# Optimization experiments

Hardware: AMD Instinct MI355X
Metric: run time of the kernel (lower is better)

## Reference

```python
import jax, jax.numpy as jnp
import numpy as np

N = 4096   # num_agents
F = 512    # feat_dim
P = 512    # phi_dim
A = 512    # aggr_dim
S = 6      # state_dim
H = 20     # MLP hidden width (hidden_layers=(20,20))


def _lstm(X, wih, whh, b):
    # torch.nn.LSTM single layer on an unbatched sequence X: [T, in] -> [T, hidden]
    pre = X @ wih + b  # [T, 4*hidden]
    Fh = whh.shape[0]
    def step(carry, p):
        h, c = carry
        g = p + h @ whh
        i, f, gg, o = jnp.split(g, 4, axis=-1)  # torch gate order: i, f, g, o
        c = jax.nn.sigmoid(f) * c + jax.nn.sigmoid(i) * jnp.tanh(gg)
        h = jax.nn.sigmoid(o) * jnp.tanh(c)
        return (h, c), h
    init = (jnp.zeros((Fh,), X.dtype), jnp.zeros((Fh,), X.dtype))
    _, hs = jax.lax.scan(step, init, pre)
    return hs


def setup_inputs():
    key = jax.random.key(0)
    ks = jax.random.split(key, 30)
    def rn(k, shape, s=0.05):
        return (jax.random.normal(k, shape) * s).astype(jnp.float32)
    x = jax.random.normal(ks[0], (N, F), dtype=jnp.float32)
    states = jax.random.normal(ks[1], (N, S), dtype=jnp.float32)
    # one comm link per agent (E == N, required by update()'s concat with x)
    src = jax.random.randint(ks[2], (N,), 0, N)
    dst = jnp.arange(N)
    inp = dict(x=x, states=states, src=src, dst=dst)
    inp["phi_w0"] = rn(ks[3], (4, F + S, H)); inp["phi_b0"] = rn(ks[4], (4, H))
    inp["phi_w1"] = rn(ks[5], (4, H, H));     inp["phi_b1"] = rn(ks[6], (4, H))
    inp["phi_w2"] = rn(ks[7], (4, H, P));     inp["phi_b2"] = rn(ks[8], (4, P))
    inp["tq_w"] = rn(ks[9], (4, P, A));  inp["tq_b"] = rn(ks[10], (4, A))
    inp["tk_w"] = rn(ks[11], (4, P, A)); inp["tk_b"] = rn(ks[12], (4, A))
    inp["tv_w"] = rn(ks[13], (4, P, A)); inp["tv_b"] = rn(ks[14], (4, A))
    inp["ts_w"] = rn(ks[15], (4, P, A)); inp["ts_b"] = rn(ks[16], (4, A))
    inp["wih0"] = rn(ks[17], (4, A + F, 4 * F)); inp["whh0"] = rn(ks[18], (4, F, 4 * F))
    inp["b0"] = rn(ks[19], (4, 4 * F))
    inp["wih1"] = rn(ks[20], (4, F, 4 * F)); inp["whh1"] = rn(ks[21], (4, F, 4 * F))
    inp["b1"] = rn(ks[22], (4, 4 * F))
    inp["cbf_w"] = rn(ks[23], (F, 1)); inp["cbf_b"] = rn(ks[24], (1,))
    return inp


def reference(x, states, src, dst, phi_w0, phi_b0, phi_w1, phi_b1, phi_w2, phi_b2,
              tq_w, tq_b, tk_w, tk_b, tv_w, tv_b, ts_w, ts_b,
              wih0, whh0, b0, wih1, whh1, b1, cbf_w, cbf_b):
    inv_sqrt_a = 1.0 / jnp.sqrt(jnp.float32(A))

    def gnn_layer(l, xin):
        # message: phi(concat(x_j, states_j - states_i))  (j = src, i = dst)
        msg = jnp.concatenate([xin[src], states[src] - states[dst]], axis=1)  # [E, F+S]
        h = jax.nn.relu(msg @ phi_w0[l] + phi_b0[l])
        h = jax.nn.relu(h @ phi_w1[l] + phi_b1[l])
        phi = h @ phi_w2[l] + phi_b2[l]  # [E, P]
        # aggregate: TransformerConv over message rows (E == N), heads=1
        q = phi @ tq_w[l] + tq_b[l]
        k = phi @ tk_w[l] + tk_b[l]
        v = phi @ tv_w[l] + tv_b[l]
        logits = jnp.sum(q[dst] * k[src], axis=-1) * inv_sqrt_a  # [E]
        m = jax.ops.segment_max(logits, dst, num_segments=N)
        e = jnp.exp(logits - m[dst])
        ssum = jax.ops.segment_sum(e, dst, num_segments=N)
        alpha = e / ssum[dst]
        aggr = jax.ops.segment_sum(alpha[:, None] * v[src], dst, num_segments=N)
        aggr = aggr + phi @ ts_w[l] + ts_b[l]  # root/skip connection
        # update: 2-layer LSTM over agents as an unbatched sequence
        gi = jnp.concatenate([aggr, xin], axis=1)  # [N, A+F]
        h0 = _lstm(gi, wih0[l], whh0[l], b0[l])
        h1 = _lstm(h0, wih1[l], whh1[l], b1[l])
        return h1

    xcur = gnn_layer(0, x)
    xcur = jax.nn.relu(xcur)
    xcur = gnn_layer(1, xcur)
    xcur = gnn_layer(2, xcur)      # feat_transformer layer 1
    xcur = jax.nn.relu(xcur)
    xcur = gnn_layer(3, xcur)      # feat_transformer layer 2
    hcbf = jax.nn.relu(xcur) @ cbf_w + cbf_b  # feat_2_CBF
    return xcur, hcbf
```

## Files before the change

### kernel.cpp

```cpp
#include <hip/hip_runtime.h>
#include <hip/hip_bf16.h>
#include <math.h>

#define NA   4096
#define FDIM 512
#define SDIM 6
#define HID  20
#define GDIM 2048
#define LWG  32

typedef unsigned long long u64;

__device__ __forceinline__ float sigf(float x) { return 1.0f / (1.0f + __expf(-x)); }
__device__ __forceinline__ float tanh_fast(float x) {
    float e = __expf(2.0f * x);
    return 1.0f - 2.0f / (e + 1.0f);
}

__device__ __forceinline__ void barrier_lds() {
    asm volatile("s_waitcnt lgkmcnt(0)\n\ts_barrier" ::: "memory");
}

__device__ __forceinline__ void atomicMaxF(float* addr, float v) {
    if (v >= 0.0f) atomicMax((int*)addr, __float_as_int(v));
    else           atomicMin((unsigned int*)addr, __float_as_uint(v));
}

__global__ void __launch_bounds__(256)
phi_fused(const float* __restrict__ xin, const float* __restrict__ states,
          const int* __restrict__ src, const int* __restrict__ dst,
          const float* __restrict__ w0, const float* __restrict__ b0,
          const float* __restrict__ w1, const float* __restrict__ b1,
          const float* __restrict__ w2, const float* __restrict__ b2,
          float* __restrict__ phi)
{
    int e = blockIdx.x, tid = threadIdx.x;
    __shared__ float msgv[FDIM + SDIM];
    __shared__ float red[240];
    __shared__ float hb1[HID];
    __shared__ float hb2[HID];
    int s = src[e], d = dst[e];
    for (int i = tid; i < FDIM; i += 256) msgv[i] = xin[(size_t)s * FDIM + i];
    if (tid < SDIM) msgv[FDIM + tid] = states[s * SDIM + tid] - states[d * SDIM + tid];
    __syncthreads();
    if (tid < 240) {
        int col = tid / 12, sg = tid % 12;
        int k0 = sg * 44, k1 = min(FDIM + SDIM, k0 + 44);
        float acc = 0.0f;
        for (int k = k0; k < k1; k++) acc += msgv[k] * w0[k * HID + col];
        red[tid] = acc;
    }
    __syncthreads();
    if (tid < HID) {
        float a = b0[tid];
#pragma unroll
        for (int q = 0; q < 12; q++) a += red[tid * 12 + q];
        hb1[tid] = fmaxf(a, 0.0f);
    }
    __syncthreads();
    if (tid < HID) {
        float a = b1[tid];
#pragma unroll
        for (int k = 0; k < HID; k++) a += hb1[k] * w1[k * HID + tid];
        hb2[tid] = fmaxf(a, 0.0f);
    }
    __syncthreads();
    for (int c = tid; c < FDIM; c += 256) {
        float a = b2[c];
#pragma unroll
        for (int k = 0; k < HID; k++) a += hb2[k] * w2[k * FDIM + c];
        phi[(size_t)e * FDIM + c] = a;
    }
}

struct Ptrs4 {
    const float* B[4];
    const float* bias[4];
    float* C[4];
};

__global__ void __launch_bounds__(256)
gemm128(const float* __restrict__ A1, int lda1,
        const float* __restrict__ A2, int lda2, int splitA,
        Ptrs4 p, int M, int N, int K)
{
    __shared__ float a_lds[16][132];
    __shared__ float b_lds[16][132];
    const float* __restrict__ B    = p.B[blockIdx.z];
    const float* __restrict__ bias = p.bias[blockIdx.z];
    float* __restrict__ C          = p.C[blockIdx.z];
    const int tid = threadIdx.x;
    const int m0 = blockIdx.y * 128, n0 = blockIdx.x * 128;
    const int ar = tid >> 2, ak4 = (tid & 3) * 4;
    const int br = tid >> 5, bc4 = (tid & 31) * 4;
    const int ty = tid >> 4, tx = tid & 15;
    float acc[8][8] = {};

    for (int kt = 0; kt < K; kt += 16) {
        int ak = kt + ak4;
        if (ak < splitA) {
            const float* r0 = A1 + (size_t)(m0 + ar) * lda1 + ak;
            const float* r1 = A1 + (size_t)(m0 + ar + 64) * lda1 + ak;
            float4 a0 = *(const float4*)r0;
            float4 a1 = *(const float4*)r1;
            a_lds[ak4 + 0][ar] = a0.x; a_lds[ak4 + 1][ar] = a0.y;
            a_lds[ak4 + 2][ar] = a0.z; a_lds[ak4 + 3][ar] = a0.w;
            a_lds[ak4 + 0][ar + 64] = a1.x; a_lds[ak4 + 1][ar + 64] = a1.y;
            a_lds[ak4 + 2][ar + 64] = a1.z; a_lds[ak4 + 3][ar + 64] = a1.w;
        } else {
            int acol = ak - splitA;
            const float* r0 = A2 + (size_t)(m0 + ar) * lda2 + acol;
            const float* r1 = A2 + (size_t)(m0 + ar + 64) * lda2 + acol;
            float4 a0 = *(const float4*)r0;
            float4 a1 = *(const float4*)r1;
            a_lds[ak4 + 0][ar] = a0.x; a_lds[ak4 + 1][ar] = a0.y;
            a_lds[ak4 + 2][ar] = a0.z; a_lds[ak4 + 3][ar] = a0.w;
            a_lds[ak4 + 0][ar + 64] = a1.x; a_lds[ak4 + 1][ar + 64] = a1.y;
            a_lds[ak4 + 2][ar + 64] = a1.z; a_lds[ak4 + 3][ar + 64] = a1.w;
        }
        {
            float4 b0v = *(const float4*)(B + (size_t)(kt + br) * N + n0 + bc4);
            float4 b1v = *(const float4*)(B + (size_t)(kt + br + 8) * N + n0 + bc4);
            *(float4*)&b_lds[br][bc4] = b0v;
            *(float4*)&b_lds[br + 8][bc4] = b1v;
        }
        __syncthreads();
#pragma unroll
        for (int kk = 0; kk < 16; kk++) {
            float av[8], bv[8];
            *(float4*)&av[0] = *(const float4*)&a_lds[kk][ty * 4];
            *(float4*)&av[4] = *(const float4*)&a_lds[kk][64 + ty * 4];
            *(float4*)&bv[0] = *(const float4*)&b_lds[kk][tx * 4];
            *(float4*)&bv[4] = *(const float4*)&b_lds[kk][64 + tx * 4];
#pragma unroll
            for (int i = 0; i < 8; i++)
#pragma unroll
                for (int j = 0; j < 8; j++)
                    acc[i][j] += av[i] * bv[j];
        }
        __syncthreads();
    }

    float4 bb0 = *(const float4*)(bias + n0 + tx * 4);
    float4 bb1 = *(const float4*)(bias + n0 + 64 + tx * 4);
    const float bbs0[4] = { bb0.x, bb0.y, bb0.z, bb0.w };
    const float bbs1[4] = { bb1.x, bb1.y, bb1.z, bb1.w };
#pragma unroll
    for (int i = 0; i < 8; i++) {
        int row = m0 + ((i < 4) ? (ty * 4 + i) : (64 + ty * 4 + i - 4));
        float4 o0, o1;
        o0.x = acc[i][0] + bbs0[0]; o0.y = acc[i][1] + bbs0[1];
        o0.z = acc[i][2] + bbs0[2]; o0.w = acc[i][3] + bbs0[3];
        o1.x = acc[i][4] + bbs1[0]; o1.y = acc[i][5] + bbs1[1];
        o1.z = acc[i][6] + bbs1[2]; o1.w = acc[i][7] + bbs1[3];
        *(float4*)&C[(size_t)row * N + n0 + tx * 4] = o0;
        *(float4*)&C[(size_t)row * N + n0 + 64 + tx * 4] = o1;
    }
}

__global__ void att_init(float* __restrict__ m, float* __restrict__ ssum)
{
    int i = blockIdx.x * blockDim.x + threadIdx.x;
    if (i < NA) { m[i] = -INFINITY; ssum[i] = 0.0f; }
}

__global__ void att_logits(const float* __restrict__ q, const float* __restrict__ k,
                           const int* __restrict__ src, const int* __restrict__ dst,
                           float* __restrict__ logits, float* __restrict__ m)
{
    int e = blockIdx.x, tid = threadIdx.x;
    int s = src[e], d = dst[e];
    const float4* qr = (const float4*)(q + (size_t)d * FDIM);
    const float4* kr = (const float4*)(k + (size_t)s * FDIM);
    float acc = 0.0f;
    for (int i = tid; i < FDIM / 4; i += 64) {
        float4 a = qr[i], b = kr[i];
        acc += a.x * b.x + a.y * b.y + a.z * b.z + a.w * b.w;
    }
    for (int off = 32; off; off >>= 1) acc += __shfl_down(acc, off);
    if (tid == 0) {
        float v = acc * 0.04419417382415922f;
        logits[e] = v;
        atomicMaxF(&m[d], v);
    }
}

__global__ void att_expsum(const float* __restrict__ logits, const float* __restrict__ m,
                           const int* __restrict__ dst,
                           float* __restrict__ ebuf, float* __restrict__ ssum)
{
    int e = blockIdx.x * blockDim.x + threadIdx.x;
    if (e < NA) {
        float v = __expf(logits[e] - m[dst[e]]);
        ebuf[e] = v;
        atomicAdd(&ssum[dst[e]], v);
    }
}

__global__ void att_scatter(const float* __restrict__ v, const int* __restrict__ src,
                            const int* __restrict__ dst, const float* __restrict__ ebuf,
                            const float* __restrict__ ssum, float* __restrict__ aggr)
{
    int e = blockIdx.x, tid = threadIdx.x;
    int s = src[e], d = dst[e];
    float alpha = ebuf[e] / ssum[d];
    const float* vr = v + (size_t)s * FDIM;
    float* ar = aggr + (size_t)d * FDIM;
    for (int c = tid; c < FDIM; c += 256) atomicAdd(&ar[c], alpha * vr[c]);
}

__global__ void __launch_bounds__(512, 2)
lstm_pair(const float* __restrict__ pre0, const float* __restrict__ whh0,
          const float* __restrict__ wih1, const float* __restrict__ whh1,
          const float* __restrict__ b1,
          float* __restrict__ xout,
          u64* __restrict__ hfull,
          u64* __restrict__ hbuf1,
          unsigned int tag0, unsigned int tag1, int T)
{
    const int wg = blockIdx.x;
    const bool roleB = wg >= LWG;
    const int w = wg & (LWG - 1);
    const int tid = threadIdx.x;
    const int lane = tid & 63;
    const int wv = tid >> 6;
    const int c = lane & 7;
    const int seg = lane >> 3;
    const int gate = c >> 1;
    const int dimoff = c & 1;
    const int hd = w * 16 + wv * 2 + dimoff;
    const int j = gate * 512 + hd;
    const bool selfWord = (tid >> 4) == w;

    __shared__ float buf[2][1088];
    __shared__ float hstage[16];
    for (int i = tid; i < 1088; i += 512) { buf[0][i] = 0.0f; buf[1][i] = 0.0f; }

    float wreg[128];
    if (!roleB) {
        const float* wc = whh0 + (size_t)(seg * 64) * GDIM + j;
#pragma unroll
        for (int kk = 0; kk < 64; kk++) wreg[kk] = wc[(size_t)kk * GDIM];
    } else {
#pragma unroll
        for (int kk = 0; kk < 128; kk++) {
            int k = seg * 128 + kk;
            wreg[kk] = (k < 512) ? wih1[(size_t)k * GDIM + j]
                                 : whh1[(size_t)(k - 512) * GDIM + j];
        }
    }
    __syncthreads();

    const int gbase = (lane & 56) | dimoff;

    if (!roleB) {
        float cst = 0.0f;
        float pre_nxt = pre0[j];
        int p = 0;
        for (int t = 0; t < T; t++) {
            const float* hb = &buf[p][seg * 68];
            float a0 = 0, a1 = 0, a2 = 0, a3 = 0;
#pragma unroll
            for (int kk = 0; kk < 64; kk += 4) {
                float4 hv = *(const float4*)(hb + kk);
                a0 += wreg[kk + 0] * hv.x;
                a1 += wreg[kk + 1] * hv.y;
                a2 += wreg[kk + 2] * hv.z;
                a3 += wreg[kk + 3] * hv.w;
            }
            float tot = (a0 + a1) + (a2 + a3);
            tot += __shfl_xor(tot, 8);
            tot += __shfl_xor(tot, 16);
            tot += __shfl_xor(tot, 32);
            tot += pre_nxt;
            if (t + 1 < T) pre_nxt = pre0[(size_t)(t + 1) * GDIM + j];
            float nl = (gate == 2) ? tanh_fast(tot) : sigf(tot);
            float ff = __shfl(nl, gbase | 2);
            float gg = __shfl(nl, gbase | 4);
            float oo = __shfl(nl, gbase | 6);
            if (lane < 2) {
                cst = ff * cst + nl * gg;
                hstage[wv * 2 + lane] = oo * tanh_fast(cst);
            }
            barrier_lds();
            if (tid < 16) {
                u64 word = ((u64)(tag0 + (unsigned)t + 1u) << 32) |
                           (u64)__float_as_uint(hstage[tid]);
                __hip_atomic_store(&hfull[(size_t)t * 512 + w * 16 + tid], word,
                                   __ATOMIC_RELAXED, __HIP_MEMORY_SCOPE_AGENT);
            }
            if (t + 1 < T) {
                float hv_;
                if (selfWord) {
                    hv_ = hstage[tid & 15];
                } else {
                    u64 want = tag0 + (unsigned)t + 1u;
                    const u64* pp = &hfull[(size_t)t * 512 + tid];
                    u64 v = __hip_atomic_load(pp, __ATOMIC_RELAXED, __HIP_MEMORY_SCOPE_AGENT);
                    while ((v >> 32) != want)
                        v = __hip_atomic_load(pp, __ATOMIC_RELAXED, __HIP_MEMORY_SCOPE_AGENT);
                    hv_ = __uint_as_float((unsigned)v);
                }
                buf[p ^ 1][(tid >> 6) * 68 + (tid & 63)] = hv_;
                barrier_lds();
                p ^= 1;
            }
        }
    } else {
        float cst = 0.0f;
        float bias = b1[j];
        int p = 0;
        {
            u64 want = tag0 + 1u;
            const u64* pp = &hfull[tid];
            u64 v = __hip_atomic_load(pp, __ATOMIC_RELAXED, __HIP_MEMORY_SCOPE_AGENT);
            while ((v >> 32) != want)
                v = __hip_atomic_load(pp, __ATOMIC_RELAXED, __HIP_MEMORY_SCOPE_AGENT);
            buf[0][(tid >> 6) * 68 + (tid & 63)] = __uint_as_float((unsigned)v);
            barrier_lds();
        }
        for (int t = 0; t < T; t++) {
            const float* hb = &buf[p][seg * 136];
            float a0 = 0, a1 = 0, a2 = 0, a3 = 0;
#pragma unroll
            for (int kk = 0; kk < 64; kk += 4) {
                float4 hv = *(const float4*)(hb + kk);
                a0 += wreg[kk + 0] * hv.x;
                a1 += wreg[kk + 1] * hv.y;
                a2 += wreg[kk + 2] * hv.z;
                a3 += wreg[kk + 3] * hv.w;
            }
#pragma unroll
            for (int kk = 0; kk < 64; kk += 4) {
                float4 hv = *(const float4*)(hb + 68 + kk);
                a0 += wreg[64 + kk + 0] * hv.x;
                a1 += wreg[64 + kk + 1] * hv.y;
                a2 += wreg[64 + kk + 2] * hv.z;
                a3 += wreg[64 + kk + 3] * hv.w;
            }
            float tot = (a0 + a1) + (a2 + a3);
            tot += __shfl_xor(tot, 8);
            tot += __shfl_xor(tot, 16);
            tot += __shfl_xor(tot, 32);
            tot += bias;
            float nl = (gate == 2) ? tanh_fast(tot) : sigf(tot);
            float ff = __shfl(nl, gbase | 2);
            float gg = __shfl(nl, gbase | 4);
            float oo = __shfl(nl, gbase | 6);
            if (lane < 2) {
                cst = ff * cst + nl * gg;
                hstage[wv * 2 + lane] = oo * tanh_fast(cst);
            }
            barrier_lds();
            if (tid < 16) {
                float h = hstage[tid];
                u64 word = ((u64)(tag1 + (unsigned)t + 1u) << 32) |
                           (u64)__float_as_uint(h);
                __hip_atomic_store(&hbuf1[(t & 1) * 512 + w * 16 + tid], word,
                                   __ATOMIC_RELAXED, __HIP_MEMORY_SCOPE_AGENT);
                xout[(size_t)t * 512 + w * 16 + tid] = h;
            }
            if (t + 1 < T) {
                float h0v, h1v;
                {
                    u64 want = tag0 + (unsigned)(t + 1) + 1u;
                    const u64* pp = &hfull[(size_t)(t + 1) * 512 + tid];
                    u64 v = __hip_atomic_load(pp, __ATOMIC_RELAXED, __HIP_MEMORY_SCOPE_AGENT);
                    while ((v >> 32) != want)
                        v = __hip_atomic_load(pp, __ATOMIC_RELAXED, __HIP_MEMORY_SCOPE_AGENT);
                    h0v = __uint_as_float((unsigned)v);
                }
                if (selfWord) {
                    h1v = hstage[tid & 15];
                } else {
                    u64 want = tag1 + (unsigned)t + 1u;
                    const u64* pp = &hbuf1[(t & 1) * 512 + tid];
                    u64 v = __hip_atomic_load(pp, __ATOMIC_RELAXED, __HIP_MEMORY_SCOPE_AGENT);
                    while ((v >> 32) != want)
                        v = __hip_atomic_load(pp, __ATOMIC_RELAXED, __HIP_MEMORY_SCOPE_AGENT);
                    h1v = __uint_as_float((unsigned)v);
                }
                buf[p ^ 1][(tid >> 6) * 68 + (tid & 63)] = h0v;
                buf[p ^ 1][(8 + (tid >> 6)) * 68 + (tid & 63)] = h1v;
                barrier_lds();
                p ^= 1;
            }
        }
    }
}

__global__ void relu_ip(float* __restrict__ x, int n)
{
    int i = blockIdx.x * blockDim.x + threadIdx.x;
    if (i < n) x[i] = fmaxf(x[i], 0.0f);
}

__global__ void cbf_head(const float* __restrict__ xc, const float* __restrict__ w,
                         const float* __restrict__ b, float* __restrict__ out)
{
    int i = blockIdx.x, tid = threadIdx.x;
    const float* xr = xc + (size_t)i * FDIM;
    float acc = 0.0f;
    for (int d = tid; d < FDIM; d += 64) acc += fmaxf(xr[d], 0.0f) * w[d];
    for (int off = 32; off; off >>= 1) acc += __shfl_down(acc, off);
    if (tid == 0) out[i] = acc + b[0];
}

__global__ void zero_u64(u64* __restrict__ p, int n)
{
    int i = blockIdx.x * blockDim.x + threadIdx.x;
    int stride = gridDim.x * blockDim.x;
    for (; i < n; i += stride) p[i] = 0ull;
}

extern "C" void kernel_launch(void* const* d_in, const int* in_sizes, int n_in,
                              void* d_out, int out_size, void* d_ws, size_t ws_size,
                              hipStream_t stream)
{
    const float* x      = (const float*)d_in[0];
    const float* states = (const float*)d_in[1];
    const int*   src    = (const int*)d_in[2];
    const int*   dst    = (const int*)d_in[3];
    const float* phi_w0 = (const float*)d_in[4];
    const float* phi_b0 = (const float*)d_in[5];
    const float* phi_w1 = (const float*)d_in[6];
    const float* phi_b1 = (const float*)d_in[7];
    const float* phi_w2 = (const float*)d_in[8];
    const float* phi_b2 = (const float*)d_in[9];
    const float* tq_w = (const float*)d_in[10]; const float* tq_b = (const float*)d_in[11];
    const float* tk_w = (const float*)d_in[12]; const float* tk_b = (const float*)d_in[13];
    const float* tv_w = (const float*)d_in[14]; const float* tv_b = (const float*)d_in[15];
    const float* ts_w = (const float*)d_in[16]; const float* ts_b = (const float*)d_in[17];
    const float* wih0 = (const float*)d_in[18]; const float* whh0 = (const float*)d_in[19];
    const float* b0   = (const float*)d_in[20];
    const float* wih1 = (const float*)d_in[21]; const float* whh1 = (const float*)d_in[22];
    const float* b1   = (const float*)d_in[23];
    const float* cbf_w = (const float*)d_in[24]; const float* cbf_b = (const float*)d_in[25];

    float* ws = (float*)d_ws;
    size_t off = 0;
    auto alloc = [&](size_t n) { float* p = ws + off; off += n; return p; };
    float* xA     = alloc((size_t)NA * FDIM);
    float* xB     = alloc((size_t)NA * FDIM);
    float* phi    = alloc((size_t)NA * FDIM);
    float* qb     = alloc((size_t)NA * FDIM);
    float* kb     = alloc((size_t)NA * FDIM);
    float* vb     = alloc((size_t)NA * FDIM);
    float* aggr   = alloc((size_t)NA * FDIM);
    float* pre    = alloc((size_t)NA * GDIM);
    float* logits = alloc(NA);
    float* mb     = alloc(NA);
    float* ssum   = alloc(NA);
    float* ebuf   = alloc(NA);
    const int HFULL_WORDS = NA * 512;
    u64* hfull = (u64*)alloc((size_t)2 * (HFULL_WORDS + 1024));
    u64* hbuf1 = hfull + HFULL_WORDS;

    float* out_x   = (float*)d_out;
    float* out_cbf = out_x + (size_t)NA * FDIM;

    zero_u64<<<2048, 256, 0, stream>>>(hfull, HFULL_WORDS + 1024);

    const float* xin = x;
    for (int l = 0; l < 4; l++) {
        float* xout = (l == 3) ? out_x : ((l & 1) ? xB : xA);

        phi_fused<<<NA, 256, 0, stream>>>(xin, states, src, dst,
            phi_w0 + (size_t)l * 518 * HID, phi_b0 + l * HID,
            phi_w1 + (size_t)l * HID * HID, phi_b1 + l * HID,
            phi_w2 + (size_t)l * HID * FDIM, phi_b2 + l * FDIM, phi);

        {
            Ptrs4 p;
            p.B[0] = tq_w + (size_t)l * FDIM * FDIM; p.bias[0] = tq_b + l * FDIM; p.C[0] = qb;
            p.B[1] = tk_w + (size_t)l * FDIM * FDIM; p.bias[1] = tk_b + l * FDIM; p.C[1] = kb;
            p.B[2] = tv_w + (size_t)l * FDIM * FDIM; p.bias[2] = tv_b + l * FDIM; p.C[2] = vb;
            p.B[3] = ts_w + (size_t)l * FDIM * FDIM; p.bias[3] = ts_b + l * FDIM; p.C[3] = aggr;
            gemm128<<<dim3(FDIM / 128, NA / 128, 4), 256, 0, stream>>>(
                phi, FDIM, phi, FDIM, FDIM, p, NA, FDIM, FDIM);
        }

        att_init<<<NA / 256, 256, 0, stream>>>(mb, ssum);
        att_logits<<<NA, 64, 0, stream>>>(qb, kb, src, dst, logits, mb);
        att_expsum<<<NA / 256, 256, 0, stream>>>(logits, mb, dst, ebuf, ssum);
        att_scatter<<<NA, 256, 0, stream>>>(vb, src, dst, ebuf, ssum, aggr);

        {
            Ptrs4 p;
            p.B[0] = wih0 + (size_t)l * 1024 * GDIM; p.bias[0] = b0 + (size_t)l * GDIM; p.C[0] = pre;
            p.B[1] = p.B[0]; p.bias[1] = p.bias[0]; p.C[1] = pre;
            p.B[2] = p.B[0]; p.bias[2] = p.bias[0]; p.C[2] = pre;
            p.B[3] = p.B[0]; p.bias[3] = p.bias[0]; p.C[3] = pre;
            gemm128<<<dim3(GDIM / 128, NA / 128, 1), 256, 0, stream>>>(
                aggr, FDIM, xin, FDIM, FDIM, p, NA, GDIM, 1024);
        }

        lstm_pair<<<2 * LWG, 512, 0, stream>>>(pre,
            whh0 + (size_t)l * FDIM * GDIM,
            wih1 + (size_t)l * FDIM * GDIM,
            whh1 + (size_t)l * FDIM * GDIM,
            b1 + (size_t)l * GDIM,
            xout, hfull, hbuf1,
            (unsigned)(2 * l) * NA, (unsigned)(2 * l + 1) * NA, NA);

        if (l == 0 || l == 2)
            relu_ip<<<(NA * FDIM + 255) / 256, 256, 0, stream>>>(xout, NA * FDIM);
        xin = xout;
    }

    cbf_head<<<NA, 64, 0, stream>>>(out_x, cbf_w, cbf_b, out_cbf);
}
```

Before: 32.45 ms.

## Unroll spin polls, raise wave priority, split stores, fuse relu into LSTM

Replaces the single-load spin loops in the persistent LSTM kernel with a four-load unrolled poll, so more loads are in flight while waiting on cross-workgroup hidden-state flags. Wave 0 gets raised scheduling priority, and the layer-1 flag store and the output store are split across two different waves. The layer-1 and hfull flag loads are now issued together before either is waited on. The separate ReLU pass is folded into the LSTM output write, removing one elementwise kernel launch and its memory traffic for two of the four layers. The extra polls add memory traffic while spinning.

```diff
diff --git a/kernel.cpp b/kernel.cpp
--- a/kernel.cpp
+++ b/kernel.cpp
@@ -19,6 +19,19 @@
 
 __device__ __forceinline__ void barrier_lds() {
     asm volatile("s_waitcnt lgkmcnt(0)\n\ts_barrier" ::: "memory");
+}
+
+__device__ __forceinline__ u64 poll4(const u64* p, unsigned want) {
+    for (;;) {
+        u64 a = __hip_atomic_load(p, __ATOMIC_RELAXED, __HIP_MEMORY_SCOPE_AGENT);
+        u64 b = __hip_atomic_load(p, __ATOMIC_RELAXED, __HIP_MEMORY_SCOPE_AGENT);
+        u64 c = __hip_atomic_load(p, __ATOMIC_RELAXED, __HIP_MEMORY_SCOPE_AGENT);
+        u64 d = __hip_atomic_load(p, __ATOMIC_RELAXED, __HIP_MEMORY_SCOPE_AGENT);
+        if ((unsigned)(a >> 32) == want) return a;
+        if ((unsigned)(b >> 32) == want) return b;
+        if ((unsigned)(c >> 32) == want) return c;
+        if ((unsigned)(d >> 32) == want) return d;
+    }
 }
 
 __device__ __forceinline__ void atomicMaxF(float* addr, float v) {
@@ -216,7 +229,7 @@
           float* __restrict__ xout,
           u64* __restrict__ hfull,
           u64* __restrict__ hbuf1,
-          unsigned int tag0, unsigned int tag1, int T)
+          unsigned int tag0, unsigned int tag1, int T, int do_relu)
 {
     const int wg = blockIdx.x;
     const bool roleB = wg >= LWG;
@@ -251,6 +264,8 @@
     }
     __syncthreads();
 
+    if (wv == 0) __builtin_amdgcn_s_setprio(1);
+
     const int gbase = (lane & 56) | dimoff;
 
     if (!roleB) {
@@ -294,11 +309,10 @@
                 if (selfWord) {
                     hv_ = hstage[tid & 15];
                 } else {
-                    u64 want = tag0 + (unsigned)t + 1u;
+                    unsigned want = tag0 + (unsigned)t + 1u;
                     const u64* pp = &hfull[(size_t)t * 512 + tid];
                     u64 v = __hip_atomic_load(pp, __ATOMIC_RELAXED, __HIP_MEMORY_SCOPE_AGENT);
-                    while ((v >> 32) != want)
-                        v = __hip_atomic_load(pp, __ATOMIC_RELAXED, __HIP_MEMORY_SCOPE_AGENT);
+                    if ((unsigned)(v >> 32) != want) v = poll4(pp, want);
                     hv_ = __uint_as_float((unsigned)v);
                 }
                 buf[p ^ 1][(tid >> 6) * 68 + (tid & 63)] = hv_;
@@ -311,11 +325,10 @@
         float bias = b1[j];
         int p = 0;
         {
-            u64 want = tag0 + 1u;
+            unsigned want = tag0 + 1u;
             const u64* pp = &hfull[tid];
             u64 v = __hip_atomic_load(pp, __ATOMIC_RELAXED, __HIP_MEMORY_SCOPE_AGENT);
-            while ((v >> 32) != want)
-                v = __hip_atomic_load(pp, __ATOMIC_RELAXED, __HIP_MEMORY_SCOPE_AGENT);
+            if ((unsigned)(v >> 32) != want) v = poll4(pp, want);
             buf[0][(tid >> 6) * 68 + (tid & 63)] = __uint_as_float((unsigned)v);
             barrier_lds();
         }
@@ -352,33 +365,35 @@
                 hstage[wv * 2 + lane] = oo * tanh_fast(cst);
             }
             barrier_lds();
-            if (tid < 16) {
-                float h = hstage[tid];
+            if (wv == 0 && lane < 16) {
+                float h = hstage[lane];
                 u64 word = ((u64)(tag1 + (unsigned)t + 1u) << 32) |
                            (u64)__float_as_uint(h);
-                __hip_atomic_store(&hbuf1[(t & 1) * 512 + w * 16 + tid], word,
+                __hip_atomic_store(&hbuf1[(t & 1) * 512 + w * 16 + lane], word,
                                    __ATOMIC_RELAXED, __HIP_MEMORY_SCOPE_AGENT);
-                xout[(size_t)t * 512 + w * 16 + tid] = h;
+            }
+            if (wv == 1 && lane < 16) {
+                float h = hstage[lane];
+                if (do_relu) h = fmaxf(h, 0.0f);
+                xout[(size_t)t * 512 + w * 16 + lane] = h;
             }
             if (t + 1 < T) {
                 float h0v, h1v;
-                {
-                    u64 want = tag0 + (unsigned)(t + 1) + 1u;
-                    const u64* pp = &hfull[(size_t)(t + 1) * 512 + tid];
-                    u64 v = __hip_atomic_load(pp, __ATOMIC_RELAXED, __HIP_MEMORY_SCOPE_AGENT);
-                    while ((v >> 32) != want)
-                        v = __hip_atomic_load(pp, __ATOMIC_RELAXED, __HIP_MEMORY_SCOPE_AGENT);
-                    h0v = __uint_as_float((unsigned)v);
-                }
+                unsigned want1 = tag1 + (unsigned)t + 1u;
+                unsigned want0 = tag0 + (unsigned)t + 2u;
+                const u64* p1 = &hbuf1[(size_t)(t & 1) * 512 + tid];
+                const u64* p0 = &hfull[(size_t)(t + 1) * 512 + tid];
+                u64 v1 = 0;
+                if (!selfWord)
+                    v1 = __hip_atomic_load(p1, __ATOMIC_RELAXED, __HIP_MEMORY_SCOPE_AGENT);
+                u64 v0 = __hip_atomic_load(p0, __ATOMIC_RELAXED, __HIP_MEMORY_SCOPE_AGENT);
+                if ((unsigned)(v0 >> 32) != want0) v0 = poll4(p0, want0);
+                h0v = __uint_as_float((unsigned)v0);
                 if (selfWord) {
                     h1v = hstage[tid & 15];
                 } else {
-                    u64 want = tag1 + (unsigned)t + 1u;
-                    const u64* pp = &hbuf1[(t & 1) * 512 + tid];
-                    u64 v = __hip_atomic_load(pp, __ATOMIC_RELAXED, __HIP_MEMORY_SCOPE_AGENT);
-                    while ((v >> 32) != want)
-                        v = __hip_atomic_load(pp, __ATOMIC_RELAXED, __HIP_MEMORY_SCOPE_AGENT);
-                    h1v = __uint_as_float((unsigned)v);
+                    if ((unsigned)(v1 >> 32) != want1) v1 = poll4(p1, want1);
+                    h1v = __uint_as_float((unsigned)v1);
                 }
                 buf[p ^ 1][(tid >> 6) * 68 + (tid & 63)] = h0v;
                 buf[p ^ 1][(8 + (tid >> 6)) * 68 + (tid & 63)] = h1v;
@@ -387,12 +402,6 @@
             }
         }
     }
-}
-
-__global__ void relu_ip(float* __restrict__ x, int n)
-{
-    int i = blockIdx.x * blockDim.x + threadIdx.x;
-    if (i < n) x[i] = fmaxf(x[i], 0.0f);
 }
 
 __global__ void cbf_head(const float* __restrict__ xc, const float* __restrict__ w,
@@ -501,10 +510,9 @@
             whh1 + (size_t)l * FDIM * GDIM,
             b1 + (size_t)l * GDIM,
             xout, hfull, hbuf1,
-            (unsigned)(2 * l) * NA, (unsigned)(2 * l + 1) * NA, NA);
-
-        if (l == 0 || l == 2)
-            relu_ip<<<(NA * FDIM + 255) / 256, 256, 0, stream>>>(xout, NA * FDIM);
+            (unsigned)(2 * l) * NA, (unsigned)(2 * l + 1) * NA, NA,
+            (l == 0 || l == 2) ? 1 : 0);
+
         xin = xout;
     }
 
```

After: 35.65 ms. 9.9% more time.
